# Performance work log

Measured on AMD Instinct MI355X. Metric: run time of the kernel, lower is better.

Reference implementation:

```python
import jax, jax.numpy as jnp
import numpy as np
import math

EMBED_DIM = 1024
NUM_HEADS = 16
HEAD_DIM = EMBED_DIM // NUM_HEADS


def setup_inputs() -> dict:
    key = jax.random.key(0)
    ks = jax.random.split(key, 9)
    B, S, D = 4, 2048, EMBED_DIM
    s = 1.0 / math.sqrt(D)
    x = jax.random.normal(ks[0], (B, S, D), dtype=jnp.float32)
    Wq = jax.random.normal(ks[1], (D, D), dtype=jnp.float32) * s
    bq = jnp.zeros((D,), dtype=jnp.float32)
    Wk = jax.random.normal(ks[2], (D, D), dtype=jnp.float32) * s
    bk = jnp.zeros((D,), dtype=jnp.float32)
    Wv = jax.random.normal(ks[3], (D, D), dtype=jnp.float32) * s
    bv = jnp.zeros((D,), dtype=jnp.float32)
    Wo = jax.random.normal(ks[4], (D, D), dtype=jnp.float32) * s
    bo = jnp.zeros((D,), dtype=jnp.float32)
    return {"x": x, "Wq": Wq, "bq": bq, "Wk": Wk, "bk": bk,
            "Wv": Wv, "bv": bv, "Wo": Wo, "bo": bo}


def reference(x, Wq, bq, Wk, bk, Wv, bv, Wo, bo):
    B, S, D = x.shape
    H, hd = NUM_HEADS, HEAD_DIM
    # projections: [B,S,D] -> [B,H,S,hd]
    def split_heads(t):
        return t.reshape(B, S, H, hd).transpose(0, 2, 1, 3)
    Q = split_heads(x @ Wq + bq)
    K = split_heads(x @ Wk + bk)
    V = split_heads(x @ Wv + bv)
    scale = 1.0 / math.sqrt(hd)
    scores = jnp.einsum('bhqd,bhkd->bhqk', Q, K) * scale  # [B,H,S,S]
    causal = jnp.tril(jnp.ones((S, S), dtype=bool))
    scores = jnp.where(causal, scores, -jnp.inf)
    attn = jax.nn.softmax(scores, axis=-1)
    out = jnp.einsum('bhqk,bhkd->bhqd', attn, V)  # [B,H,S,hd]
    out = out.transpose(0, 2, 1, 3).reshape(B, S, D)
    return out @ Wo + bo
```

## Files before the change

### kernel.cpp

```cpp
#include <hip/hip_runtime.h>
#include <hip/hip_bf16.h>
#include <cstdint>
#include <cstddef>

typedef __bf16 bf16_t;
typedef __bf16 bf16x4 __attribute__((ext_vector_type(4)));
typedef __bf16 bf16x8 __attribute__((ext_vector_type(8)));
typedef float f32x4 __attribute__((ext_vector_type(4)));
typedef float f32x16 __attribute__((ext_vector_type(16)));
typedef unsigned u32x2 __attribute__((ext_vector_type(2)));

typedef __attribute__((address_space(1))) void as1_void_t;
typedef __attribute__((address_space(3))) void as3_void_t;

__device__ __forceinline__ void gload_lds16(const bf16_t* g, bf16_t* l) {
  __builtin_amdgcn_global_load_lds((as1_void_t*)g, (as3_void_t*)l, 16, 0, 0);
}

__global__ __launch_bounds__(256) void prep_x_k(
    const float* __restrict__ x, bf16_t* __restrict__ xb)
{
  const int stride = gridDim.x * blockDim.x;
  const int tid = blockIdx.x * blockDim.x + threadIdx.x;
  const int NX4 = (8192 * 1024) / 4;
  for (int i = tid; i < NX4; i += stride) {
    float4 v = ((const float4*)x)[i];
    bf16x4 o;
    o[0] = (bf16_t)v.x; o[1] = (bf16_t)v.y; o[2] = (bf16_t)v.z; o[3] = (bf16_t)v.w;
    ((bf16x4*)xb)[i] = o;
  }
}

__global__ __launch_bounds__(256) void prep_w_k(
    const float* __restrict__ wq, const float* __restrict__ wk,
    const float* __restrict__ wv, const float* __restrict__ wo,
    bf16_t* __restrict__ wqt, bf16_t* __restrict__ wkt,
    bf16_t* __restrict__ wvt, bf16_t* __restrict__ wot)
{
  __shared__ float t[64][65];
  const int zz = blockIdx.y;
  const float* w = (zz == 0) ? wq : (zz == 1) ? wk : (zz == 2) ? wv : wo;
  bf16_t* wt = (zz == 0) ? wqt : (zz == 1) ? wkt : (zz == 2) ? wvt : wot;
  const int tile = blockIdx.x;
  const int tr = tile >> 4, tc = tile & 15;
  const int c = threadIdx.x & 63, r4 = threadIdx.x >> 6;
#pragma unroll
  for (int rr = 0; rr < 16; ++rr) {
    int row = rr * 4 + r4;
    t[row][c] = w[(size_t)(tr * 64 + row) * 1024 + tc * 64 + c];
  }
  __syncthreads();
#pragma unroll
  for (int rr = 0; rr < 16; ++rr) {
    int row = rr * 4 + r4;
    wt[(size_t)(tc * 64 + row) * 1024 + tr * 64 + c] = (bf16_t)t[c][row];
  }
}

constexpr int BM = 128, BN = 128, BK = 64;

__global__ __launch_bounds__(256) void gemm_qkv_k(
    const bf16_t* __restrict__ A,
    const bf16_t* __restrict__ WqT, const bf16_t* __restrict__ WkT,
    const bf16_t* __restrict__ WvT,
    const float* __restrict__ bq, const float* __restrict__ bk,
    const float* __restrict__ bv,
    bf16_t* __restrict__ qo, bf16_t* __restrict__ ko, bf16_t* __restrict__ vo)
{
  constexpr int K = 1024;
  __shared__ bf16_t a_lds[BM * BK];
  __shared__ bf16_t b_lds[BN * BK];
  const int z = blockIdx.z;
  const bf16_t* Bt = (z == 0) ? WqT : (z == 1) ? WkT : WvT;
  const float* bias = (z == 0) ? bq : (z == 1) ? bk : bv;
  bf16_t* outp = (z == 0) ? qo : (z == 1) ? ko : vo;
  const float oscale = (z == 0) ? 0.18033688011112042f : 1.0f;

  const int tid = threadIdx.x;
  const int l = tid & 63;
  const int wv = tid >> 6;
  const int wr = wv >> 1, wc = wv & 1;
  const int lr = l & 15, lg = l >> 4;
  const int bm = blockIdx.x * BM;
  const int bn = blockIdx.y * BN;

  f32x4 acc[4][4] = {};

  const int srow = tid >> 3;
  const int scc = tid & 7;

  for (int k0 = 0; k0 < K; k0 += BK) {
    __syncthreads();
#pragma unroll
    for (int it = 0; it < 4; ++it) {
      int row = srow + it * 32;
      int gk = (scc ^ (row & 7)) * 8;
      gload_lds16(A + (size_t)(bm + row) * K + k0 + gk, a_lds + row * BK + scc * 8);
      gload_lds16(Bt + (size_t)(bn + row) * K + k0 + gk, b_lds + row * BK + scc * 8);
    }
    __syncthreads();
#pragma unroll
    for (int kk = 0; kk < 2; ++kk) {
      bf16x8 af[4], bfr[4];
#pragma unroll
      for (int m = 0; m < 4; ++m) {
        int row = wr * 64 + m * 16 + lr;
        int ch = (kk * 4 + lg) ^ (row & 7);
        af[m] = *(const bf16x8*)&a_lds[row * BK + ch * 8];
      }
#pragma unroll
      for (int n = 0; n < 4; ++n) {
        int row = wc * 64 + n * 16 + lr;
        int ch = (kk * 4 + lg) ^ (row & 7);
        bfr[n] = *(const bf16x8*)&b_lds[row * BK + ch * 8];
      }
#pragma unroll
      for (int m = 0; m < 4; ++m)
#pragma unroll
        for (int n = 0; n < 4; ++n)
          acc[m][n] = __builtin_amdgcn_mfma_f32_16x16x32_bf16(af[m], bfr[n], acc[m][n], 0, 0, 0);
    }
  }

#pragma unroll
  for (int m = 0; m < 4; ++m) {
#pragma unroll
    for (int n = 0; n < 4; ++n) {
#pragma unroll
      for (int r = 0; r < 4; ++r) {
        int row = bm + wr * 64 + m * 16 + lg * 4 + r;
        int col = bn + wc * 64 + n * 16 + lr;
        float v = acc[m][n][r] + bias[col];
        if (z < 2) {
          outp[((size_t)((row >> 11) * 16 + (col >> 6)) * 2048 + (row & 2047)) * 64 + (col & 63)] =
              (bf16_t)(v * oscale);
        } else {
          outp[((size_t)((row >> 11) * 16 + (col >> 6)) * 64 + (col & 63)) * 2048 + (row & 2047)] =
              (bf16_t)v;
        }
      }
    }
  }
}

__global__ __launch_bounds__(256) void gemm_o_k(
    const bf16_t* __restrict__ A, const bf16_t* __restrict__ Bt,
    const float* __restrict__ bias, float* __restrict__ outp)
{
  constexpr int K = 1024;
  __shared__ bf16_t a_lds[BM * BK];
  __shared__ bf16_t b_lds[BN * BK];
  const int tid = threadIdx.x;
  const int l = tid & 63;
  const int wv = tid >> 6;
  const int wr = wv >> 1, wc = wv & 1;
  const int lr = l & 15, lg = l >> 4;
  const int bm = blockIdx.x * BM;
  const int bn = blockIdx.y * BN;

  f32x4 acc[4][4] = {};
  const int srow = tid >> 3;
  const int scc = tid & 7;

  for (int k0 = 0; k0 < K; k0 += BK) {
    __syncthreads();
#pragma unroll
    for (int it = 0; it < 4; ++it) {
      int row = srow + it * 32;
      int gk = (scc ^ (row & 7)) * 8;
      gload_lds16(A + (size_t)(bm + row) * K + k0 + gk, a_lds + row * BK + scc * 8);
      gload_lds16(Bt + (size_t)(bn + row) * K + k0 + gk, b_lds + row * BK + scc * 8);
    }
    __syncthreads();
#pragma unroll
    for (int kk = 0; kk < 2; ++kk) {
      bf16x8 af[4], bfr[4];
#pragma unroll
      for (int m = 0; m < 4; ++m) {
        int row = wr * 64 + m * 16 + lr;
        int ch = (kk * 4 + lg) ^ (row & 7);
        af[m] = *(const bf16x8*)&a_lds[row * BK + ch * 8];
      }
#pragma unroll
      for (int n = 0; n < 4; ++n) {
        int row = wc * 64 + n * 16 + lr;
        int ch = (kk * 4 + lg) ^ (row & 7);
        bfr[n] = *(const bf16x8*)&b_lds[row * BK + ch * 8];
      }
#pragma unroll
      for (int m = 0; m < 4; ++m)
#pragma unroll
        for (int n = 0; n < 4; ++n)
          acc[m][n] = __builtin_amdgcn_mfma_f32_16x16x32_bf16(af[m], bfr[n], acc[m][n], 0, 0, 0);
    }
  }

#pragma unroll
  for (int m = 0; m < 4; ++m)
#pragma unroll
    for (int n = 0; n < 4; ++n)
#pragma unroll
      for (int r = 0; r < 4; ++r) {
        int row = bm + wr * 64 + m * 16 + lg * 4 + r;
        int col = bn + wc * 64 + n * 16 + lr;
        outp[(size_t)row * 1024 + col] = acc[m][n][r] + bias[col];
      }
}

__device__ __forceinline__ unsigned pack2bf(float a, float b) {
  union { bf16_t h[2]; unsigned u; } z;
  z.h[0] = (bf16_t)a; z.h[1] = (bf16_t)b;
  return z.u;
}

__device__ __forceinline__ void permswap(unsigned& a, unsigned& b) {
  u32x2 r = __builtin_amdgcn_permlane32_swap(a, b, false, false);
  a = r[0]; b = r[1];
}

__device__ __forceinline__ float xadd32(float x) {
  unsigned a = __float_as_uint(x), b = __float_as_uint(x);
  permswap(a, b);
  return __uint_as_float(a) + __uint_as_float(b);
}

__device__ __forceinline__ void sm_pv(
    const f32x16& st, const bf16x8 vf[2][2], f32x16 oacc[2], float& ls)
{
  float p[16];
#pragma unroll
  for (int r = 0; r < 16; ++r) p[r] = __builtin_amdgcn_exp2f(st[r] - 16.0f);
  float s0 = (p[0] + p[1]) + (p[2] + p[3]);
  float s1 = (p[4] + p[5]) + (p[6] + p[7]);
  float s2 = (p[8] + p[9]) + (p[10] + p[11]);
  float s3 = (p[12] + p[13]) + (p[14] + p[15]);
  ls += ((s0 + s1) + (s2 + s3));

  bf16x8 pf[2];
#pragma unroll
  for (int ks = 0; ks < 2; ++ks) {
    unsigned a0 = pack2bf(p[8 * ks + 0], p[8 * ks + 1]);
    unsigned a1 = pack2bf(p[8 * ks + 2], p[8 * ks + 3]);
    unsigned b0 = pack2bf(p[8 * ks + 4], p[8 * ks + 5]);
    unsigned b1 = pack2bf(p[8 * ks + 6], p[8 * ks + 7]);
    permswap(a0, b0);
    permswap(a1, b1);
    union { unsigned wd[4]; bf16x8 v; } zz;
    zz.wd[0] = a0; zz.wd[1] = a1; zz.wd[2] = b0; zz.wd[3] = b1;
    pf[ks] = zz.v;
  }
  __builtin_amdgcn_s_setprio(1);
#pragma unroll
  for (int dt = 0; dt < 2; ++dt)
#pragma unroll
    for (int ks = 0; ks < 2; ++ks)
      oacc[dt] = __builtin_amdgcn_mfma_f32_32x32x16_bf16(vf[dt][ks], pf[ks], oacc[dt], 0, 0, 0);
  __builtin_amdgcn_s_setprio(0);
}

__global__ __launch_bounds__(256) void attn_k(
    const bf16_t* __restrict__ Q, const bf16_t* __restrict__ Kmat,
    const bf16_t* __restrict__ Vt, bf16_t* __restrict__ O)
{
  const int S = 2048, HD = 64;
  const int bh = blockIdx.x;
  const int tid = threadIdx.x;
  const int l = tid & 63;
  const int w = tid >> 6;
  const int idx = blockIdx.y * 4 + w;
  const int qb1 = idx * 32, qb2 = (63 - idx) * 32;
  const int lc = l & 31;
  const int hi = l >> 5;

  const bf16_t* Qh = Q + (size_t)bh * S * HD;
  const bf16_t* Kh = Kmat + (size_t)bh * S * HD;
  const bf16_t* Vh = Vt + (size_t)bh * HD * S;

  bf16x8 qf1[4], qf2[4];
#pragma unroll
  for (int ds = 0; ds < 4; ++ds) {
    qf1[ds] = *(const bf16x8*)&Qh[(size_t)(qb1 + lc) * HD + ds * 16 + hi * 8];
    qf2[ds] = *(const bf16x8*)&Qh[(size_t)(qb2 + lc) * HD + ds * 16 + hi * 8];
  }

  float ls1 = 0.f, ls2 = 0.f;
  f32x16 o1[2] = {}, o2[2] = {};

  auto step = [&](const bf16x8 (&kf)[4], bf16x8 (&kfn)[4], int kvb) {
    bf16x8 vf[2][2];
#pragma unroll
    for (int dt = 0; dt < 2; ++dt)
#pragma unroll
      for (int ks = 0; ks < 2; ++ks)
        vf[dt][ks] = *(const bf16x8*)&Vh[(size_t)(dt * 32 + lc) * S + kvb + ks * 16 + hi * 8];
    const int kvn = (kvb + 32 <= qb2) ? kvb + 32 : kvb;
#pragma unroll
    for (int ds = 0; ds < 4; ++ds)
      kfn[ds] = *(const bf16x8*)&Kh[(size_t)(kvn + lc) * HD + ds * 16 + hi * 8];

    f32x16 st2 = {};
    __builtin_amdgcn_s_setprio(1);
#pragma unroll
    for (int ds = 0; ds < 4; ++ds)
      st2 = __builtin_amdgcn_mfma_f32_32x32x16_bf16(kf[ds], qf2[ds], st2, 0, 0, 0);
    __builtin_amdgcn_s_setprio(0);
    const bool d1 = (kvb <= qb1);
    f32x16 st1 = {};
    if (d1) {
      __builtin_amdgcn_s_setprio(1);
#pragma unroll
      for (int ds = 0; ds < 4; ++ds)
        st1 = __builtin_amdgcn_mfma_f32_32x32x16_bf16(kf[ds], qf1[ds], st1, 0, 0, 0);
      __builtin_amdgcn_s_setprio(0);
    }
    if (kvb == qb2) {
#pragma unroll
      for (int r = 0; r < 16; ++r) {
        int kvloc = (r & 3) + 8 * (r >> 2) + 4 * hi;
        if (kvloc > lc) st2[r] = -1e30f;
      }
    }
    if (d1 && kvb == qb1) {
#pragma unroll
      for (int r = 0; r < 16; ++r) {
        int kvloc = (r & 3) + 8 * (r >> 2) + 4 * hi;
        if (kvloc > lc) st1[r] = -1e30f;
      }
    }
    sm_pv(st2, vf, o2, ls2);
    if (d1) sm_pv(st1, vf, o1, ls1);
  };

  bf16x8 kfA[4], kfB[4];
#pragma unroll
  for (int ds = 0; ds < 4; ++ds)
    kfA[ds] = *(const bf16x8*)&Kh[(size_t)lc * HD + ds * 16 + hi * 8];

  int kvb = 0;
  while (true) {
    step(kfA, kfB, kvb);
    kvb += 32;
    if (kvb > qb2) break;
    step(kfB, kfA, kvb);
    kvb += 32;
    if (kvb > qb2) break;
  }

  const int b = bh >> 4, h = bh & 15;
  {
    const float inv = 1.0f / xadd32(ls1);
    const size_t rowoff = (size_t)(b * 2048 + qb1 + lc) * 1024 + h * 64;
#pragma unroll
    for (int dt = 0; dt < 2; ++dt)
#pragma unroll
      for (int g = 0; g < 4; ++g) {
        bf16x4 o4;
#pragma unroll
        for (int t = 0; t < 4; ++t) o4[t] = (bf16_t)(o1[dt][g * 4 + t] * inv);
        *(bf16x4*)&O[rowoff + dt * 32 + g * 8 + hi * 4] = o4;
      }
  }
  {
    const float inv = 1.0f / xadd32(ls2);
    const size_t rowoff = (size_t)(b * 2048 + qb2 + lc) * 1024 + h * 64;
#pragma unroll
    for (int dt = 0; dt < 2; ++dt)
#pragma unroll
      for (int g = 0; g < 4; ++g) {
        bf16x4 o4;
#pragma unroll
        for (int t = 0; t < 4; ++t) o4[t] = (bf16_t)(o2[dt][g * 4 + t] * inv);
        *(bf16x4*)&O[rowoff + dt * 32 + g * 8 + hi * 4] = o4;
      }
  }
}

extern "C" void kernel_launch(void* const* d_in, const int* in_sizes, int n_in,
                              void* d_out, int out_size, void* d_ws, size_t ws_size,
                              hipStream_t stream)
{
  (void)in_sizes; (void)n_in; (void)out_size; (void)ws_size;
  const float* x  = (const float*)d_in[0];
  const float* Wq = (const float*)d_in[1];
  const float* bq = (const float*)d_in[2];
  const float* Wk = (const float*)d_in[3];
  const float* bk = (const float*)d_in[4];
  const float* Wv = (const float*)d_in[5];
  const float* bv = (const float*)d_in[6];
  const float* Wo = (const float*)d_in[7];
  const float* bo = (const float*)d_in[8];

  char* ws = (char*)d_ws;
  bf16_t* xb   = (bf16_t*)(ws);
  bf16_t* wqt  = (bf16_t*)(ws + (size_t)(16u << 20));
  bf16_t* wkt  = (bf16_t*)(ws + (size_t)(18u << 20));
  bf16_t* wvt  = (bf16_t*)(ws + (size_t)(20u << 20));
  bf16_t* wot  = (bf16_t*)(ws + (size_t)(22u << 20));
  bf16_t* qws  = (bf16_t*)(ws + (size_t)(24u << 20));
  bf16_t* kws  = (bf16_t*)(ws + (size_t)(40u << 20));
  bf16_t* vtws = (bf16_t*)(ws + (size_t)(56u << 20));

  prep_x_k<<<2048, 256, 0, stream>>>(x, xb);
  prep_w_k<<<dim3(256, 4), 256, 0, stream>>>(Wq, Wk, Wv, Wo, wqt, wkt, wvt, wot);

  dim3 gg(8192 / BM, 1024 / BN, 3);
  gemm_qkv_k<<<gg, 256, 0, stream>>>(xb, wqt, wkt, wvt, bq, bk, bv, qws, kws, vtws);

  attn_k<<<dim3(64, 8), 256, 0, stream>>>(qws, kws, vtws, xb);

  dim3 go(8192 / BM, 1024 / BN);
  gemm_o_k<<<go, 256, 0, stream>>>(xb, wot, bo, (float*)d_out);
}
```

Measured before the change: 210.9 us.

## Store Q/K/V in MFMA-fragment-swizzled layout for contiguous attention loads

The QKV projection epilogue now writes Q, K and V^T into a tiled layout where each 32-row tile's MFMA operand fragments are laid out per lane. The attention kernel can then load each fragment as one contiguous 16-byte-per-lane chunk instead of strided row loads. This is meant to cut uncoalesced global load traffic in the attention inner loop. In exchange the projection epilogue does scattered 2-byte stores with more index arithmetic, which could slow that GEMM.

```diff
diff --git a/kernel.cpp b/kernel.cpp
--- a/kernel.cpp
+++ b/kernel.cpp
@@ -131,12 +131,18 @@
         int row = bm + wr * 64 + m * 16 + lg * 4 + r;
         int col = bn + wc * 64 + n * 16 + lr;
         float v = acc[m][n][r] + bias[col];
+        const int bh = (row >> 11) * 16 + (col >> 6);
+        const int seq = row & 2047;
+        const int d = col & 63;
         if (z < 2) {
-          outp[((size_t)((row >> 11) * 16 + (col >> 6)) * 2048 + (row & 2047)) * 64 + (col & 63)] =
-              (bf16_t)(v * oscale);
+          size_t off = (((size_t)(bh * 64 + (seq >> 5)) * 4 + (d >> 4)) * 64
+                        + (((d >> 3) & 1) * 32 + (seq & 31))) * 8 + (d & 7);
+          outp[off] = (bf16_t)(v * oscale);
         } else {
-          outp[((size_t)((row >> 11) * 16 + (col >> 6)) * 64 + (col & 63)) * 2048 + (row & 2047)] =
-              (bf16_t)v;
+          size_t off = ((((size_t)(bh * 64 + (seq >> 5)) * 2 + (d >> 5)) * 2
+                         + ((seq >> 4) & 1)) * 64
+                        + (((seq >> 3) & 1) * 32 + (d & 31))) * 8 + (seq & 7);
+          outp[off] = (bf16_t)v;
         }
       }
     }
@@ -262,41 +268,41 @@
     const bf16_t* __restrict__ Q, const bf16_t* __restrict__ Kmat,
     const bf16_t* __restrict__ Vt, bf16_t* __restrict__ O)
 {
-  const int S = 2048, HD = 64;
   const int bh = blockIdx.x;
   const int tid = threadIdx.x;
   const int l = tid & 63;
   const int w = tid >> 6;
   const int idx = blockIdx.y * 4 + w;
-  const int qb1 = idx * 32, qb2 = (63 - idx) * 32;
+  const int t1 = idx, t2 = 63 - idx;
+  const int qb1 = t1 * 32, qb2 = t2 * 32;
   const int lc = l & 31;
   const int hi = l >> 5;
 
-  const bf16_t* Qh = Q + (size_t)bh * S * HD;
-  const bf16_t* Kh = Kmat + (size_t)bh * S * HD;
-  const bf16_t* Vh = Vt + (size_t)bh * HD * S;
+  const bf16_t* Qh = Q + (size_t)bh * 131072 + l * 8;
+  const bf16_t* Kh = Kmat + (size_t)bh * 131072 + l * 8;
+  const bf16_t* Vh = Vt + (size_t)bh * 131072 + l * 8;
 
   bf16x8 qf1[4], qf2[4];
 #pragma unroll
   for (int ds = 0; ds < 4; ++ds) {
-    qf1[ds] = *(const bf16x8*)&Qh[(size_t)(qb1 + lc) * HD + ds * 16 + hi * 8];
-    qf2[ds] = *(const bf16x8*)&Qh[(size_t)(qb2 + lc) * HD + ds * 16 + hi * 8];
+    qf1[ds] = *(const bf16x8*)&Qh[(size_t)(t1 * 4 + ds) * 512];
+    qf2[ds] = *(const bf16x8*)&Qh[(size_t)(t2 * 4 + ds) * 512];
   }
 
   float ls1 = 0.f, ls2 = 0.f;
   f32x16 o1[2] = {}, o2[2] = {};
 
-  auto step = [&](const bf16x8 (&kf)[4], bf16x8 (&kfn)[4], int kvb) {
+  auto step = [&](const bf16x8 (&kf)[4], bf16x8 (&kfn)[4], int kvt) {
+    const bf16_t* vb = &Vh[(size_t)kvt * 2048];
     bf16x8 vf[2][2];
-#pragma unroll
-    for (int dt = 0; dt < 2; ++dt)
-#pragma unroll
-      for (int ks = 0; ks < 2; ++ks)
-        vf[dt][ks] = *(const bf16x8*)&Vh[(size_t)(dt * 32 + lc) * S + kvb + ks * 16 + hi * 8];
-    const int kvn = (kvb + 32 <= qb2) ? kvb + 32 : kvb;
+    vf[0][0] = *(const bf16x8*)&vb[0];
+    vf[0][1] = *(const bf16x8*)&vb[512];
+    vf[1][0] = *(const bf16x8*)&vb[1024];
+    vf[1][1] = *(const bf16x8*)&vb[1536];
+    const int kvn = (kvt + 1 <= t2) ? kvt + 1 : kvt;
 #pragma unroll
     for (int ds = 0; ds < 4; ++ds)
-      kfn[ds] = *(const bf16x8*)&Kh[(size_t)(kvn + lc) * HD + ds * 16 + hi * 8];
+      kfn[ds] = *(const bf16x8*)&Kh[(size_t)(kvn * 4 + ds) * 512];
 
     f32x16 st2 = {};
     __builtin_amdgcn_s_setprio(1);
@@ -304,7 +310,7 @@
     for (int ds = 0; ds < 4; ++ds)
       st2 = __builtin_amdgcn_mfma_f32_32x32x16_bf16(kf[ds], qf2[ds], st2, 0, 0, 0);
     __builtin_amdgcn_s_setprio(0);
-    const bool d1 = (kvb <= qb1);
+    const bool d1 = (kvt <= t1);
     f32x16 st1 = {};
     if (d1) {
       __builtin_amdgcn_s_setprio(1);
@@ -313,14 +319,14 @@
         st1 = __builtin_amdgcn_mfma_f32_32x32x16_bf16(kf[ds], qf1[ds], st1, 0, 0, 0);
       __builtin_amdgcn_s_setprio(0);
     }
-    if (kvb == qb2) {
+    if (kvt == t2) {
 #pragma unroll
       for (int r = 0; r < 16; ++r) {
         int kvloc = (r & 3) + 8 * (r >> 2) + 4 * hi;
         if (kvloc > lc) st2[r] = -1e30f;
       }
     }
-    if (d1 && kvb == qb1) {
+    if (d1 && kvt == t1) {
 #pragma unroll
       for (int r = 0; r < 16; ++r) {
         int kvloc = (r & 3) + 8 * (r >> 2) + 4 * hi;
@@ -334,16 +340,16 @@
   bf16x8 kfA[4], kfB[4];
 #pragma unroll
   for (int ds = 0; ds < 4; ++ds)
-    kfA[ds] = *(const bf16x8*)&Kh[(size_t)lc * HD + ds * 16 + hi * 8];
-
-  int kvb = 0;
+    kfA[ds] = *(const bf16x8*)&Kh[(size_t)ds * 512];
+
+  int kvt = 0;
   while (true) {
-    step(kfA, kfB, kvb);
-    kvb += 32;
-    if (kvb > qb2) break;
-    step(kfB, kfA, kvb);
-    kvb += 32;
-    if (kvb > qb2) break;
+    step(kfA, kfB, kvt);
+    ++kvt;
+    if (kvt > t2) break;
+    step(kfB, kfA, kvt);
+    ++kvt;
+    if (kvt > t2) break;
   }
 
   const int b = bh >> 4, h = bh & 15;
```

After: 198.9 us. 1.06x faster.
